# Optimization experiments

Measured on AMD Instinct MI355X. Metric: run time of the kernel, lower is better.

The kernel has to match this reference:

```python
import jax, jax.numpy as jnp
import numpy as np

NUM_EMB = 8192
EMB_DIM = 512
COMMITMENT_COST = 0.25
TEMPERATURE = 1.0
ENTROPY_WEIGHT = 0.1


def setup_inputs() -> dict:
    key = jax.random.key(0)
    k1, k2 = jax.random.split(key)
    z = jax.random.normal(k1, (32768, EMB_DIM), dtype=jnp.float32)
    W = jax.random.normal(k2, (NUM_EMB, EMB_DIM), dtype=jnp.float32) * 0.1
    return {"z": z, "W": W}


def reference(z, W):
    # pairwise squared distances [B, K] (scaled by temperature)
    distances = (jnp.sum(z * z, axis=1, keepdims=True)
                 + jnp.sum(W * W, axis=1)
                 - 2.0 * z @ W.T) / TEMPERATURE
    indices = jnp.argmin(distances, axis=1)          # [B]
    quantized = W[indices]                            # [B, D] gather

    commitment_loss = jnp.mean((z - jax.lax.stop_gradient(quantized)) ** 2)
    codebook_loss = jnp.mean((quantized - jax.lax.stop_gradient(z)) ** 2)

    # entropy loss over code assignment histogram
    counts = jnp.zeros((NUM_EMB,), jnp.float32).at[indices].add(1.0)
    probs = counts / jnp.maximum(counts.sum(), 1.0)
    entropy = -jnp.sum(probs * jnp.log(probs + 1e-10))
    max_entropy = jnp.log(jnp.float32(NUM_EMB))
    entropy_loss = 1.0 - entropy / max_entropy

    loss = codebook_loss + COMMITMENT_COST * commitment_loss + ENTROPY_WEIGHT * entropy_loss

    # straight-through estimator
    quantized_st = z + jax.lax.stop_gradient(quantized - z)
    return quantized_st, loss, indices
```

## Files before the change

kernel.cpp:

```cpp
#include <hip/hip_runtime.h>
#include <math.h>

#define B_ROWS 32768
#define D_DIM  512
#define K_EMB  8192

#define BMT 128
#define BNT 128
#define RSPLIT 16
#define KRANGE_R (K_EMB / RSPLIT)
#define EPS 0.10f

typedef __attribute__((ext_vector_type(4))) float f32x4;
typedef __attribute__((ext_vector_type(8))) short bf16x8;

#define GLL16(gp, lp)                                                          \
  __builtin_amdgcn_global_load_lds(                                            \
      (const __attribute__((address_space(1))) void*)(gp),                     \
      (__attribute__((address_space(3))) void*)(lp), 16, 0, 0)

__device__ __forceinline__ unsigned bf_rne(float x) {
  unsigned u = __float_as_uint(x);
  return (u + 0x7fffu + ((u >> 16) & 1u)) >> 16;
}

__global__ __launch_bounds__(256) void prep_kernel(
    const float* __restrict__ X, short* __restrict__ hi,
    short* __restrict__ lo, float* __restrict__ sq, int nrows) {
  const int wave = threadIdx.x >> 6;
  const int lane = threadIdx.x & 63;
  const int row = blockIdx.x * 4 + wave;
  if (row >= nrows) return;
  const float* xr = X + (size_t)row * D_DIM;
  float4 x0 = ((const float4*)xr)[lane * 2];
  float4 x1 = ((const float4*)xr)[lane * 2 + 1];
  float xs[8] = {x0.x, x0.y, x0.z, x0.w, x1.x, x1.y, x1.z, x1.w};
  union { short s[8]; int4 v; } H, L;
  float ssum = 0.f;
  #pragma unroll
  for (int j = 0; j < 8; ++j) {
    unsigned rh = bf_rne(xs[j]);
    H.s[j] = (short)rh;
    float h = __uint_as_float(rh << 16);
    L.s[j] = (short)bf_rne(xs[j] - h);
    ssum += xs[j] * xs[j];
  }
  *(int4*)(hi + (size_t)row * D_DIM + lane * 8) = H.v;
  *(int4*)(lo + (size_t)row * D_DIM + lane * 8) = L.v;
  #pragma unroll
  for (int o = 32; o > 0; o >>= 1) ssum += __shfl_xor(ssum, o, 64);
  if (lane == 0) sq[row] = ssum;
}

__global__ __launch_bounds__(512, 4) void stage1_kernel(
    const short* __restrict__ zhi, const short* __restrict__ whi,
    const float* __restrict__ wsq, float* __restrict__ cv1,
    int* __restrict__ ci1, float* __restrict__ cv2) {
  __shared__ short Zt[32768];
  float* rv1 = (float*)Zt;
  int*   ri1 = (int*)(Zt + 1024);
  float* rv2 = (float*)(Zt + 2048);

  const int tid = threadIdx.x;
  const int lane = tid & 63;
  const int wave = tid >> 6;
  const int l15 = lane & 15, l4 = lane >> 4;
  const int row0 = blockIdx.x * 64;

  #pragma unroll
  for (int j = 0; j < 8; ++j) {
    const int slot = j * 512 + tid;
    const int r = slot & 63, dc = slot >> 6;
    GLL16(zhi + (size_t)(row0 + r) * D_DIM + dc * 8, Zt + (size_t)slot * 8);
  }

  const short* pb[2];
  #pragma unroll
  for (int cb = 0; cb < 2; ++cb)
    pb[cb] = whi + (size_t)(wave * 32 + cb * 16 + l15) * D_DIM + l4 * 8;

  float v1[16], v2[16];
  int   i1[16];
  #pragma unroll
  for (int s = 0; s < 16; ++s) { v1[s] = INFINITY; v2[s] = INFINITY; i1[s] = 0x7fffffff; }

  bf16x8 bcur[2];
  #pragma unroll
  for (int cb = 0; cb < 2; ++cb) bcur[cb] = *(const bf16x8*)(pb[cb]);

  __syncthreads();

  for (int kt = 0; kt < K_EMB; kt += 256) {
    f32x4 acc[4][2];
    #pragma unroll
    for (int rb = 0; rb < 4; ++rb)
      #pragma unroll
      for (int cb = 0; cb < 2; ++cb) acc[rb][cb] = (f32x4)0.f;

    #pragma unroll 4
    for (int dc = 0; dc < 16; ++dc) {
      const int nt0 = (dc == 15) ? kt + 256 : kt;
      const int nt = (nt0 < K_EMB) ? nt0 : 0;
      const int nd = (dc == 15) ? 0 : (dc + 1) * 32;
      const size_t noff = (size_t)nt * D_DIM + nd;
      bf16x8 bnxt[2];
      #pragma unroll
      for (int cb = 0; cb < 2; ++cb) bnxt[cb] = *(const bf16x8*)(pb[cb] + noff);

      bf16x8 a[4];
      #pragma unroll
      for (int rb = 0; rb < 4; ++rb)
        a[rb] = *(const bf16x8*)&Zt[((dc * 4 + l4) * 64 + rb * 16 + l15) * 8];
      #pragma unroll
      for (int rb = 0; rb < 4; ++rb)
        #pragma unroll
        for (int cb = 0; cb < 2; ++cb)
          acc[rb][cb] = __builtin_amdgcn_mfma_f32_16x16x32_bf16(
              a[rb], bcur[cb], acc[rb][cb], 0, 0, 0);
      #pragma unroll
      for (int cb = 0; cb < 2; ++cb) bcur[cb] = bnxt[cb];
    }

    #pragma unroll
    for (int cb = 0; cb < 2; ++cb) {
      const int col = kt + wave * 32 + cb * 16 + l15;
      const float wv = wsq[col];
      #pragma unroll
      for (int rb = 0; rb < 4; ++rb) {
        f32x4 a = acc[rb][cb];
        #pragma unroll
        for (int rg = 0; rg < 4; ++rg) {
          const float dist = wv - 2.0f * a[rg];
          const int s = rb * 4 + rg;
          if (dist < v1[s]) {
            v2[s] = v1[s]; v1[s] = dist; i1[s] = col;
          } else {
            v2[s] = fminf(v2[s], dist);
          }
        }
      }
    }
  }

  __syncthreads();
  #pragma unroll
  for (int s = 0; s < 16; ++s) {
    float a1 = v1[s], a2 = v2[s];
    int ai = i1[s];
    #pragma unroll
    for (int m = 1; m < 16; m <<= 1) {
      const float b1 = __shfl_xor(a1, m, 64);
      const float b2 = __shfl_xor(a2, m, 64);
      const int   bi = __shfl_xor(ai, m, 64);
      if (b1 < a1 || (b1 == a1 && bi < ai)) {
        a2 = fminf(a1, b2); a1 = b1; ai = bi;
      } else {
        a2 = fminf(a2, b1);
      }
    }
    if (l15 == 0) {
      const int r = (s >> 2) * 16 + l4 * 4 + (s & 3);
      rv1[r * 8 + wave] = a1;
      ri1[r * 8 + wave] = ai;
      rv2[r * 8 + wave] = a2;
    }
  }
  __syncthreads();

  if (tid < 64) {
    float V1 = INFINITY, V2 = INFINITY;
    int I1 = 0x7fffffff;
    #pragma unroll
    for (int w = 0; w < 8; ++w) {
      const float a1 = rv1[tid * 8 + w];
      const int ai = ri1[tid * 8 + w];
      const float a2 = rv2[tid * 8 + w];
      if (a1 < V1 || (a1 == V1 && ai < I1)) {
        V2 = fminf(V1, a2); V1 = a1; I1 = ai;
      } else {
        V2 = fminf(V2, a1);
      }
    }
    cv1[row0 + tid] = V1; ci1[row0 + tid] = I1; cv2[row0 + tid] = V2;
  }
}

__global__ __launch_bounds__(256) void merge_flag_kernel(
    const float* __restrict__ cv1, const int* __restrict__ ci1,
    const float* __restrict__ cv2, int* __restrict__ idx,
    float* __restrict__ out_idx_f, int* __restrict__ hist,
    unsigned long long* __restrict__ packed, int* __restrict__ cnt,
    int* __restrict__ list) {
  const int row = blockIdx.x * 256 + threadIdx.x;
  const float V1 = cv1[row];
  const int I1 = ci1[row];
  const float V2 = cv2[row];
  if (V2 - V1 >= EPS) {
    idx[row] = I1;
    out_idx_f[row] = (float)I1;
    atomicAdd(&hist[I1], 1);
  } else {
    packed[row] = 0xffffffffffffffffULL;
    const int p = atomicAdd(cnt, 1);
    list[p] = row;
  }
}

__global__ __launch_bounds__(256, 2) void refine_kernel(
    const short* __restrict__ zhi, const short* __restrict__ zlo,
    const short* __restrict__ whi, const short* __restrict__ wlo,
    const float* __restrict__ zz, const float* __restrict__ wsq,
    const int* __restrict__ cnt, const int* __restrict__ list,
    unsigned long long* __restrict__ packed) {
  __shared__ char smem[32768];
  short* Ah = (short*)smem;
  short* Al = (short*)(smem + 8192);
  short* Bh = (short*)(smem + 16384);
  short* Bl = (short*)(smem + 24576);
  float* rv = (float*)smem;
  int*   ri = (int*)(smem + 16384);

  const int n = *cnt;
  const int bx = blockIdx.x;
  const int rt = bx >> 4;
  const int ks = bx & 15;
  if (rt * BMT >= n) return;
  const int k0 = ks * KRANGE_R;

  const int tid = threadIdx.x;
  const int lane = tid & 63;
  const int wave = tid >> 6;
  const int wm = wave >> 1, wn = wave & 1;
  const int l15 = lane & 15, l4 = lane >> 4;

  const int r0s = tid & 127;
  const int kc0 = tid >> 7;
  const int kc1 = kc0 + 2;
  const int rowg = list[min(rt * BMT + r0s, n - 1)];

  float zzr[16];
  #pragma unroll
  for (int rb = 0; rb < 4; ++rb)
    #pragma unroll
    for (int rg = 0; rg < 4; ++rg) {
      const int m = wm * 64 + rb * 16 + l4 * 4 + rg;
      zzr[rb * 4 + rg] = zz[list[min(rt * BMT + m, n - 1)]];
    }

  float best[16];
  int   bidx[16];
  #pragma unroll
  for (int s = 0; s < 16; ++s) { best[s] = INFINITY; bidx[s] = 0x7fffffff; }

  for (int kt = 0; kt < KRANGE_R; kt += BNT) {
    f32x4 acc[4][4];
    #pragma unroll
    for (int rb = 0; rb < 4; ++rb)
      #pragma unroll
      for (int cb = 0; cb < 4; ++cb) acc[rb][cb] = (f32x4)0.f;

    for (int d0 = 0; d0 < D_DIM; d0 += 32) {
      const size_t ga0 = (size_t)rowg * D_DIM + d0 + kc0 * 8;
      const size_t ga1 = (size_t)rowg * D_DIM + d0 + kc1 * 8;
      const size_t gb0 = (size_t)(k0 + kt + r0s) * D_DIM + d0 + kc0 * 8;
      const size_t gb1 = (size_t)(k0 + kt + r0s) * D_DIM + d0 + kc1 * 8;
      GLL16(zhi + ga0, Ah + (size_t)tid * 8);
      GLL16(zhi + ga1, Ah + (size_t)(tid + 256) * 8);
      GLL16(zlo + ga0, Al + (size_t)tid * 8);
      GLL16(zlo + ga1, Al + (size_t)(tid + 256) * 8);
      GLL16(whi + gb0, Bh + (size_t)tid * 8);
      GLL16(whi + gb1, Bh + (size_t)(tid + 256) * 8);
      GLL16(wlo + gb0, Bl + (size_t)tid * 8);
      GLL16(wlo + gb1, Bl + (size_t)(tid + 256) * 8);
      __syncthreads();

      bf16x8 ah[4], al[4], bh[4], bl[4];
      #pragma unroll
      for (int rb = 0; rb < 4; ++rb) {
        const int m = wm * 64 + rb * 16 + l15;
        ah[rb] = *(const bf16x8*)&Ah[(l4 * 128 + m) * 8];
        al[rb] = *(const bf16x8*)&Al[(l4 * 128 + m) * 8];
      }
      #pragma unroll
      for (int cb = 0; cb < 4; ++cb) {
        const int nn = wn * 64 + cb * 16 + l15;
        bh[cb] = *(const bf16x8*)&Bh[(l4 * 128 + nn) * 8];
        bl[cb] = *(const bf16x8*)&Bl[(l4 * 128 + nn) * 8];
      }
      #pragma unroll
      for (int rb = 0; rb < 4; ++rb)
        #pragma unroll
        for (int cb = 0; cb < 4; ++cb) {
          acc[rb][cb] = __builtin_amdgcn_mfma_f32_16x16x32_bf16(
              ah[rb], bh[cb], acc[rb][cb], 0, 0, 0);
          acc[rb][cb] = __builtin_amdgcn_mfma_f32_16x16x32_bf16(
              ah[rb], bl[cb], acc[rb][cb], 0, 0, 0);
          acc[rb][cb] = __builtin_amdgcn_mfma_f32_16x16x32_bf16(
              al[rb], bh[cb], acc[rb][cb], 0, 0, 0);
        }
      __syncthreads();
    }

    #pragma unroll
    for (int cb = 0; cb < 4; ++cb) {
      const int col = k0 + kt + wn * 64 + cb * 16 + l15;
      const float wv = wsq[col];
      #pragma unroll
      for (int rb = 0; rb < 4; ++rb) {
        f32x4 a = acc[rb][cb];
        #pragma unroll
        for (int rg = 0; rg < 4; ++rg) {
          const float dist = (zzr[rb * 4 + rg] + wv) - 2.0f * a[rg];
          const int s = rb * 4 + rg;
          if (dist < best[s]) { best[s] = dist; bidx[s] = col; }
        }
      }
    }
  }

  #pragma unroll
  for (int rb = 0; rb < 4; ++rb)
    #pragma unroll
    for (int rg = 0; rg < 4; ++rg) {
      const int s = rb * 4 + rg;
      const int R = wm * 64 + rb * 16 + l4 * 4 + rg;
      rv[R * 32 + wn * 16 + l15] = best[s];
      ri[R * 32 + wn * 16 + l15] = bidx[s];
    }
  __syncthreads();

  if (tid < BMT && rt * BMT + tid < n) {
    float bv = INFINITY;
    int bi = 0x7fffffff;
    #pragma unroll
    for (int t = 0; t < 32; ++t) {
      const float v = rv[tid * 32 + t];
      const int ix = ri[tid * 32 + t];
      if (v < bv || (v == bv && ix < bi)) { bv = v; bi = ix; }
    }
    const int row = list[rt * BMT + tid];
    const unsigned long long pk =
        ((unsigned long long)__float_as_uint(bv) << 32) | (unsigned)bi;
    atomicMin(&packed[row], pk);
  }
}

__global__ __launch_bounds__(256) void final_merge_kernel(
    const int* __restrict__ cnt, const int* __restrict__ list,
    const unsigned long long* __restrict__ packed, int* __restrict__ idx,
    float* __restrict__ out_idx_f, int* __restrict__ hist) {
  const int t = blockIdx.x * 256 + threadIdx.x;
  if (t >= *cnt) return;
  const int row = list[t];
  const int bi = (int)(packed[row] & 0xffffffffULL);
  idx[row] = bi;
  out_idx_f[row] = (float)bi;
  atomicAdd(&hist[bi], 1);
}

__global__ __launch_bounds__(256) void gather_kernel(
    const float* __restrict__ z, const float* __restrict__ W,
    const int* __restrict__ idx, float* __restrict__ out,
    double* __restrict__ mse_part) {
  __shared__ float wsum[4];
  const int wave = threadIdx.x >> 6;
  const int lane = threadIdx.x & 63;
  const int row = blockIdx.x * 4 + wave;
  const int k = idx[row];
  const float* zr = z + (size_t)row * D_DIM;
  const float* wr = W + (size_t)k * D_DIM;
  float* outr = out + (size_t)row * D_DIM;
  float s = 0.f;
  #pragma unroll
  for (int h = 0; h < 2; ++h) {
    const int c = h * 256 + lane * 4;
    float4 zv = *(const float4*)(zr + c);
    float4 qv = *(const float4*)(wr + c);
    float4 st;
    st.x = zv.x + (qv.x - zv.x);
    st.y = zv.y + (qv.y - zv.y);
    st.z = zv.z + (qv.z - zv.z);
    st.w = zv.w + (qv.w - zv.w);
    float dx = zv.x - qv.x, dy = zv.y - qv.y, dz = zv.z - qv.z, dw = zv.w - qv.w;
    s += dx * dx + dy * dy + dz * dz + dw * dw;
    *(float4*)(outr + c) = st;
  }
  #pragma unroll
  for (int o = 32; o > 0; o >>= 1) s += __shfl_xor(s, o, 64);
  if (lane == 0) wsum[wave] = s;
  __syncthreads();
  if (threadIdx.x == 0)
    mse_part[blockIdx.x] =
        (double)wsum[0] + (double)wsum[1] + (double)wsum[2] + (double)wsum[3];
}

__global__ __launch_bounds__(256) void loss_kernel(
    const int* __restrict__ hist, const double* __restrict__ mse_part,
    float* __restrict__ out_loss) {
  __shared__ float ls[4];
  __shared__ double ld[4];
  const int tid = threadIdx.x;
  float e = 0.f;
  double ms = 0.0;
  for (int b = tid; b < K_EMB; b += 256) {
    float p = (float)hist[b] * (1.0f / 32768.0f);
    e += p * logf(p + 1e-10f);
    ms += mse_part[b];
  }
  #pragma unroll
  for (int o = 32; o > 0; o >>= 1) {
    e += __shfl_xor(e, o, 64);
    ms += __shfl_xor(ms, o, 64);
  }
  if ((tid & 63) == 0) { ls[tid >> 6] = e; ld[tid >> 6] = ms; }
  __syncthreads();
  if (tid == 0) {
    float entropy = -(ls[0] + ls[1] + ls[2] + ls[3]);
    float mse = (float)((ld[0] + ld[1] + ld[2] + ld[3]) / 16777216.0);
    float entropy_loss = 1.0f - entropy / logf(8192.0f);
    out_loss[0] = mse + 0.25f * mse + 0.1f * entropy_loss;
  }
}

extern "C" void kernel_launch(void* const* d_in, const int* in_sizes, int n_in,
                              void* d_out, int out_size, void* d_ws, size_t ws_size,
                              hipStream_t stream) {
  const float* z = (const float*)d_in[0];
  const float* W = (const float*)d_in[1];
  float* out = (float*)d_out;

  char* ws = (char*)d_ws;
  int*    cnt     = (int*)(ws + 8);
  int*    hist    = (int*)(ws + 4096);
  unsigned long long* packed = (unsigned long long*)(ws + 65536);
  float*  zz   = (float*)(ws + 327680);
  float*  wsq  = (float*)(ws + 458752);
  int*    idx  = (int*)(ws + 491520);
  int*    list = (int*)(ws + 622592);
  float*  cv1  = (float*)(ws + 786432);
  int*    ci1  = (int*)(ws + 1310720);
  float*  cv2  = (float*)(ws + 1835008);
  double* mse_part = (double*)(ws + 2097152);
  short*  zhi  = (short*)(ws + 4194304);
  short*  zlo  = (short*)(ws + 37748736);
  short*  whi  = (short*)(ws + 71303168);
  short*  wlo  = (short*)(ws + 79691776);

  hipMemsetAsync(d_ws, 0, 36864, stream);

  prep_kernel<<<B_ROWS / 4, 256, 0, stream>>>(z, zhi, zlo, zz, B_ROWS);
  prep_kernel<<<K_EMB / 4, 256, 0, stream>>>(W, whi, wlo, wsq, K_EMB);

  stage1_kernel<<<B_ROWS / 64, 512, 0, stream>>>(zhi, whi, wsq, cv1, ci1, cv2);

  merge_flag_kernel<<<B_ROWS / 256, 256, 0, stream>>>(
      cv1, ci1, cv2, idx, out + (size_t)B_ROWS * D_DIM + 1, hist,
      packed, cnt, list);

  refine_kernel<<<(B_ROWS / BMT) * RSPLIT, 256, 0, stream>>>(
      zhi, zlo, whi, wlo, zz, wsq, cnt, list, packed);

  final_merge_kernel<<<B_ROWS / 256, 256, 0, stream>>>(
      cnt, list, packed, idx, out + (size_t)B_ROWS * D_DIM + 1, hist);

  gather_kernel<<<B_ROWS / 4, 256, 0, stream>>>(z, W, idx, out, mse_part);

  loss_kernel<<<1, 256, 0, stream>>>(hist, mse_part,
                                     out + (size_t)B_ROWS * D_DIM);
}
```

Measured before the change: 803.0 us.

## Deepen B-operand prefetch to three steps and stagger codebook tile order per block

```diff
diff --git a/kernel.cpp b/kernel.cpp
--- a/kernel.cpp
+++ b/kernel.cpp
@@ -66,6 +66,7 @@
   const int wave = tid >> 6;
   const int l15 = lane & 15, l4 = lane >> 4;
   const int row0 = blockIdx.x * 64;
+  const int off = ((blockIdx.x >> 3) & 7) * 4;
 
   #pragma unroll
   for (int j = 0; j < 8; ++j) {
@@ -79,51 +80,58 @@
   for (int cb = 0; cb < 2; ++cb)
     pb[cb] = whi + (size_t)(wave * 32 + cb * 16 + l15) * D_DIM + l4 * 8;
 
+  auto b_off = [&](int lg) -> size_t {
+    const int pt = ((lg >> 4) + off) & 31;
+    return (size_t)(pt * 256) * D_DIM + (size_t)((lg & 15) * 32);
+  };
+
   float v1[16], v2[16];
   int   i1[16];
   #pragma unroll
   for (int s = 0; s < 16; ++s) { v1[s] = INFINITY; v2[s] = INFINITY; i1[s] = 0x7fffffff; }
 
-  bf16x8 bcur[2];
-  #pragma unroll
-  for (int cb = 0; cb < 2; ++cb) bcur[cb] = *(const bf16x8*)(pb[cb]);
-
-  __syncthreads();
-
-  for (int kt = 0; kt < K_EMB; kt += 256) {
+  bf16x8 bp[4][2];
+  #pragma unroll
+  for (int p = 0; p < 3; ++p) {
+    const size_t o0 = b_off(p);
+    #pragma unroll
+    for (int cb = 0; cb < 2; ++cb) bp[p][cb] = *(const bf16x8*)(pb[cb] + o0);
+  }
+
+  __syncthreads();
+
+  for (int t = 0; t < 32; ++t) {
+    const int ktc = (((t + off) & 31) << 8);
     f32x4 acc[4][2];
     #pragma unroll
     for (int rb = 0; rb < 4; ++rb)
       #pragma unroll
       for (int cb = 0; cb < 2; ++cb) acc[rb][cb] = (f32x4)0.f;
 
-    #pragma unroll 4
+    #pragma unroll
     for (int dc = 0; dc < 16; ++dc) {
-      const int nt0 = (dc == 15) ? kt + 256 : kt;
-      const int nt = (nt0 < K_EMB) ? nt0 : 0;
-      const int nd = (dc == 15) ? 0 : (dc + 1) * 32;
-      const size_t noff = (size_t)nt * D_DIM + nd;
-      bf16x8 bnxt[2];
-      #pragma unroll
-      for (int cb = 0; cb < 2; ++cb) bnxt[cb] = *(const bf16x8*)(pb[cb] + noff);
-
+      const int lg = t * 16 + dc;
       bf16x8 a[4];
       #pragma unroll
       for (int rb = 0; rb < 4; ++rb)
         a[rb] = *(const bf16x8*)&Zt[((dc * 4 + l4) * 64 + rb * 16 + l15) * 8];
+      {
+        const size_t o3 = b_off(lg + 3);
+        #pragma unroll
+        for (int cb = 0; cb < 2; ++cb)
+          bp[(dc + 3) & 3][cb] = *(const bf16x8*)(pb[cb] + o3);
+      }
       #pragma unroll
       for (int rb = 0; rb < 4; ++rb)
         #pragma unroll
         for (int cb = 0; cb < 2; ++cb)
           acc[rb][cb] = __builtin_amdgcn_mfma_f32_16x16x32_bf16(
-              a[rb], bcur[cb], acc[rb][cb], 0, 0, 0);
-      #pragma unroll
-      for (int cb = 0; cb < 2; ++cb) bcur[cb] = bnxt[cb];
+              a[rb], bp[dc & 3][cb], acc[rb][cb], 0, 0, 0);
     }
 
     #pragma unroll
     for (int cb = 0; cb < 2; ++cb) {
-      const int col = kt + wave * 32 + cb * 16 + l15;
+      const int col = ktc + wave * 32 + cb * 16 + l15;
       const float wv = wsq[col];
       #pragma unroll
       for (int rb = 0; rb < 4; ++rb) {
@@ -132,7 +140,7 @@
         for (int rg = 0; rg < 4; ++rg) {
           const float dist = wv - 2.0f * a[rg];
           const int s = rb * 4 + rg;
-          if (dist < v1[s]) {
+          if (dist < v1[s] || (dist == v1[s] && col < i1[s])) {
             v2[s] = v1[s]; v1[s] = dist; i1[s] = col;
           } else {
             v2[s] = fminf(v2[s], dist);
```

Measured after the change: 2.751 ms. 3.43x slower.
